# Kernel optimization log

Measured on AMD Instinct MI355X. Metric: run time of the kernel, lower is better.

## Reference

```python
import jax, jax.numpy as jnp
import numpy as np

H, W = 256, 336
FLOW_SCALING = float(max(H, W))  # max(config['loader']['resolution'])
REG_WEIGHT = 0.001               # config['loss']['flow_regul_weight']
B, N = 8, 262144


def setup_inputs() -> dict:
    key = jax.random.key(0)
    k1, k2, k3, k4, k5 = jax.random.split(key, 5)
    # small flow so a reasonable fraction of warped events stays in-bounds
    flow = 0.05 * jax.random.normal(k1, (B, 2, H, W), dtype=jnp.float32)
    ys = jax.random.randint(k2, (B, N), 0, H).astype(jnp.float32)
    xs = jax.random.randint(k3, (B, N), 0, W).astype(jnp.float32)
    ts = jax.random.uniform(k4, (B, N), dtype=jnp.float32)  # normalized timestamps in [0,1]
    pol = jax.random.randint(k5, (B, N), 0, 2)
    # event layout per the code: (ts, y, x, p)
    event_list = jnp.stack([ts, ys, xs, pol.astype(jnp.float32) * 2.0 - 1.0], axis=-1)
    pol_mask = jnp.stack([(pol == 1), (pol == 0)], axis=-1).astype(jnp.float32)  # [B,N,2]
    return {"flow": flow, "event_list": event_list, "pol_mask": pol_mask}


def _get_interpolation(events, event_flow, tref):
    # warped event coords (y, x): [B, N, 2]
    warped = events[:, :, 1:3] + (tref - events[:, :, 0:1]) * event_flow * FLOW_SCALING
    top_y = jnp.floor(warped[:, :, 0:1])
    bot_y = jnp.floor(warped[:, :, 0:1] + 1.0)
    left_x = jnp.floor(warped[:, :, 1:2])
    right_x = jnp.floor(warped[:, :, 1:2] + 1.0)
    # four bilinear corners stacked along event dim -> [B, 4N, 2]
    idx = jnp.concatenate([
        jnp.concatenate([top_y, left_x], -1),
        jnp.concatenate([top_y, right_x], -1),
        jnp.concatenate([bot_y, left_x], -1),
        jnp.concatenate([bot_y, right_x], -1)], axis=1)
    warped4 = jnp.tile(warped, (1, 4, 1))
    weights = jnp.maximum(0.0, 1.0 - jnp.abs(warped4 - idx))
    mask = ((idx[:, :, 0:1] >= 0) & (idx[:, :, 0:1] < H)
            & (idx[:, :, 1:2] >= 0) & (idx[:, :, 1:2] < W)).astype(weights.dtype)
    idx = idx * mask          # unfeasible indices -> 0
    weights = weights * mask  # unfeasible weights -> 0
    flat_idx = (idx[:, :, 0] * W + idx[:, :, 1]).astype(jnp.int32)  # [B, 4N]
    w = jnp.prod(weights, axis=-1, keepdims=True)                    # [B, 4N, 1]
    return flat_idx, w


def _interpolate(flat_idx, weights, polarity_mask):
    # scatter-add bilinear weights into an H*W image, per batch element
    w = (weights * polarity_mask)[:, :, 0]  # [B, 4N]
    return jax.vmap(lambda i, v: jax.ops.segment_sum(v, i, num_segments=H * W))(flat_idx, w)


def reference(flow, event_list, pol_mask):
    pol4 = jnp.tile(pol_mask, (1, 4, 1))              # [B, 4N, 2]
    ts4 = jnp.tile(event_list[:, :, 0:1], (1, 4, 1))  # [B, 4N, 1]
    # gather flow at original event pixel locations
    flow_idx = (event_list[:, :, 1] * W + event_list[:, :, 2]).astype(jnp.int32)  # [B, N]
    flow_flat = flow.reshape(flow.shape[0], 2, -1)
    event_flowy = jnp.take_along_axis(flow_flat[:, 1, :], flow_idx, axis=1)
    event_flowx = jnp.take_along_axis(flow_flat[:, 0, :], flow_idx, axis=1)
    event_flow = jnp.stack([event_flowy, event_flowx], axis=-1)  # [B, N, 2] (y, x)

    loss = jnp.float32(0.0)
    # forward warp (tref=1, avg ts) and backward warp (tref=0, avg 1-ts)
    for tref, tgrad in ((1.0, ts4), (0.0, 1.0 - ts4)):
        idx, wts = _get_interpolation(event_list, event_flow, tref)
        for p in range(2):  # positive / negative polarity
            pm = pol4[:, :, p:p + 1]
            iwe = _interpolate(idx, wts, pm)
            iwe_ts = _interpolate(idx, wts * tgrad, pm)
            loss = loss + jnp.sum((iwe_ts / (iwe + 1e-9)) ** 2)

    # charbonnier flow smoothness
    flow_dx = flow[:, :, :-1, :] - flow[:, :, 1:, :]
    flow_dy = flow[:, :, :, :-1] - flow[:, :, :, 1:]
    smooth = jnp.sum(jnp.sqrt(flow_dx ** 2 + 1e-6)) + jnp.sum(jnp.sqrt(flow_dy ** 2 + 1e-6))
    return loss + REG_WEIGHT * smooth
```

## Files before the change

### kernel.cpp

```cpp
#include <hip/hip_runtime.h>

#define HH 256
#define WW 336
#define HWPIX (HH * WW)
#define BATCH 8
#define NEV 262144
#define NEV_SHIFT 18
#define FLOW_SCALING 336.0f
#define REG_WEIGHT 0.001f

#define BANDS 32
#define BANDSHIFT 3
#define BANDROWS 8
#define NBINS (2 * BATCH * BANDS)
#define CAP 14336
#define GSTRIDE 16

#define BE_THREADS 512
#define EVPT 2
#define EV_PER_BLOCK (BE_THREADS * EVPT)
#define MAXITEMS 4096

#define HTILE (BANDROWS * WW)
#define NBLK_ACC NBINS

#define GCOUNT_BYTES (NBINS * GSTRIDE * 4)
#define ITEMS_BYTES ((size_t)NBINS * CAP * 8)

__device__ __forceinline__ float wave_reduce_sum(float v) {
    #pragma unroll
    for (int o = 32; o > 0; o >>= 1) v += __shfl_down(v, o, 64);
    return v;
}

__device__ __forceinline__ float charb(float d) { return sqrtf(d * d + 1e-6f); }

__global__ __launch_bounds__(256)
void flow_prep(const float* __restrict__ flow,
               unsigned int* __restrict__ gcount, float* __restrict__ loss_acc,
               unsigned int* __restrict__ done_count,
               float* __restrict__ smooth_partial) {
    __shared__ float red[4];
    int tid = threadIdx.x;
    if (blockIdx.x == 0) {
        for (int i = tid; i < NBINS * GSTRIDE; i += 256) gcount[i] = 0u;
        if (tid == 0) { *loss_acc = 0.0f; *done_count = 0u; }
    }

    const int N4 = BATCH * HWPIX / 4;
    const int H4 = HWPIX / 4;
    const int W4 = WW / 4;
    float v = 0.0f;
    for (int i = blockIdx.x * 256 + tid; i < N4; i += gridDim.x * 256) {
        int b = i / H4, u = i - b * H4;
        int row = u / W4, c4 = u - row * W4;
        const float4* ch0 = (const float4*)(flow + (size_t)b * 2 * HWPIX);
        const float4* ch1 = ch0 + H4;
        float4 a0 = ch0[u];
        float4 a1 = ch1[u];

        if (row < HH - 1) {
            float4 d0 = ch0[u + W4];
            float4 d1 = ch1[u + W4];
            v += charb(a0.x - d0.x) + charb(a0.y - d0.y) +
                 charb(a0.z - d0.z) + charb(a0.w - d0.w) +
                 charb(a1.x - d1.x) + charb(a1.y - d1.y) +
                 charb(a1.z - d1.z) + charb(a1.w - d1.w);
        }
        v += charb(a0.x - a0.y) + charb(a0.y - a0.z) + charb(a0.z - a0.w) +
             charb(a1.x - a1.y) + charb(a1.y - a1.z) + charb(a1.z - a1.w);
        if (c4 < W4 - 1) {
            float r0 = ((const float*)ch0)[4 * u + 4];
            float r1 = ((const float*)ch1)[4 * u + 4];
            v += charb(a0.w - r0) + charb(a1.w - r1);
        }
    }
    v = wave_reduce_sum(v);
    if ((tid & 63) == 0) red[tid >> 6] = v;
    __syncthreads();
    if (tid < 4) {
        float r = red[tid];
        r += __shfl_down(r, 2, 64);
        r += __shfl_down(r, 1, 64);
        if (tid == 0) smooth_partial[blockIdx.x] = r;
    }
}

__global__ __launch_bounds__(BE_THREADS)
void bin_events(const float* __restrict__ flow,
                const float4* __restrict__ ev,
                unsigned int* __restrict__ gcount,
                uint2* __restrict__ items) {
    __shared__ int lcnt[64];
    __shared__ int loff[64];
    __shared__ int gbase[64];
    __shared__ int stotal;
    __shared__ __align__(16) unsigned long long sval[MAXITEMS];

    int tid = threadIdx.x;
    if (tid < 64) lcnt[tid] = 0;
    __syncthreads();

    int base = blockIdx.x * EV_PER_BLOCK;
    int b = base >> NEV_SHIFT;
    const float* fxp = flow + (size_t)b * 2 * HWPIX;
    const float* fyp = fxp + HWPIX;

    unsigned int pkv[EVPT][2];
    unsigned int hiA[EVPT][2], hiB[EVPT][2];
    int rkA[EVPT][2], rkB[EVPT][2];

    #pragma unroll
    for (int e = 0; e < EVPT; ++e) {
        int bn = base + e * BE_THREADS + tid;
        float4 ee = ev[bn];
        float t = ee.x, y = ee.y, x = ee.z;
        unsigned int p = (ee.w > 0.0f) ? 0u : 1u;

        int iy = (int)y, ix = (int)x;
        int off = iy * WW + ix;
        float fx = fxp[off];
        float fy = fyp[off];

        #pragma unroll
        for (int tr = 0; tr < 2; ++tr) {
            rkA[e][tr] = -1; rkB[e][tr] = -1;
            float tref  = tr ? 0.0f : 1.0f;
            float tg    = tr ? (1.0f - t) : t;
            float dtS = (tref - t) * FLOW_SCALING;
            float wy = fmaf(dtS, fy, y);
            float wx = fmaf(dtS, fx, x);
            if (!(wx > -1.0f && wx < (float)WW)) continue;
            if (!(wy > -1.0f && wy < (float)HH)) continue;

            int ty = (int)floorf(wy);
            int band0 = -1, band1 = -1;
            if (ty >= 0 && ty < HH) band0 = ty >> BANDSHIFT;
            int r1 = ty + 1;
            if (r1 >= 0 && r1 < HH) {
                int bb = r1 >> BANDSHIFT;
                if (bb != band0) band1 = bb;
            }

            unsigned int qx = (unsigned int)(fmaf(wx, 2048.0f, 2048.5f));
            unsigned int qt = (unsigned int)(tg * 2047.0f + 0.5f);
            pkv[e][tr] = (qx << 12) | (qt << 1) | p;

            if (band0 >= 0) {
                float wyrel = wy - (float)(band0 * BANDROWS - 1);
                unsigned int qy = (unsigned int)fmaf(wyrel, 2048.0f, 0.5f);
                int lb = tr * BANDS + band0;
                hiA[e][tr] = qy | ((unsigned int)lb << 16);
                rkA[e][tr] = atomicAdd(&lcnt[lb], 1);
            }
            if (band1 >= 0) {
                float wyrel = wy - (float)(band1 * BANDROWS - 1);
                unsigned int qy = (unsigned int)fmaf(wyrel, 2048.0f, 0.5f);
                int lb = tr * BANDS + band1;
                hiB[e][tr] = qy | ((unsigned int)lb << 16);
                rkB[e][tr] = atomicAdd(&lcnt[lb], 1);
            }
        }
    }
    __syncthreads();

    if (tid < 64) {
        int c = lcnt[tid];
        int xg = c;
        #pragma unroll
        for (int o = 1; o < 64; o <<= 1) {
            int yv = __shfl_up(xg, o, 64);
            if (tid >= o) xg += yv;
        }
        loff[tid] = xg - c;
        if (tid == 63) stotal = xg;
        int gbin = ((tid >> 5) * BATCH + b) * BANDS + (tid & 31);
        gbase[tid] = c > 0 ? (int)atomicAdd(&gcount[gbin * GSTRIDE],
                                            (unsigned int)c) : 0;
    }
    __syncthreads();

    #pragma unroll
    for (int e = 0; e < EVPT; ++e) {
        #pragma unroll
        for (int tr = 0; tr < 2; ++tr) {
            if (rkA[e][tr] >= 0) {
                int lb = (hiA[e][tr] >> 16) & 63;
                sval[loff[lb] + rkA[e][tr]] =
                    (unsigned long long)pkv[e][tr] |
                    ((unsigned long long)hiA[e][tr] << 32);
            }
            if (rkB[e][tr] >= 0) {
                int lb = (hiB[e][tr] >> 16) & 63;
                sval[loff[lb] + rkB[e][tr]] =
                    (unsigned long long)pkv[e][tr] |
                    ((unsigned long long)hiB[e][tr] << 32);
            }
        }
    }
    __syncthreads();

    int total = stotal;
    for (int i = tid * 2; i < total; i += 2 * BE_THREADS) {
        uint4 two = *(const uint4*)&sval[i];
        unsigned int pk0 = two.x, h0 = two.y;
        unsigned int qy0 = h0 & 0xffffu;
        int lb0 = (h0 >> 16) & 63;
        int gs0 = gbase[lb0] + (i - loff[lb0]);
        int gbin0 = ((lb0 >> 5) * BATCH + b) * BANDS + (lb0 & 31);

        if ((i + 1) < total) {
            unsigned int pk1 = two.z, h1 = two.w;
            unsigned int qy1 = h1 & 0xffffu;
            int lb1 = (h1 >> 16) & 63;
            int gs1 = gbase[lb1] + (i + 1 - loff[lb1]);
            if (lb1 == lb0 && (gs0 & 1) == 0 && gs1 < CAP) {
                *(uint4*)(items + (size_t)gbin0 * CAP + gs0) =
                    make_uint4(pk0, qy0, pk1, qy1);
                continue;
            }
            int gbin1 = ((lb1 >> 5) * BATCH + b) * BANDS + (lb1 & 31);
            if (gs1 < CAP) items[(size_t)gbin1 * CAP + gs1] = make_uint2(pk1, qy1);
        }
        if (gs0 < CAP) items[(size_t)gbin0 * CAP + gs0] = make_uint2(pk0, qy0);
    }
}

__device__ __forceinline__ unsigned int pack_w(float w, float tg) {
    unsigned int lo16 = (unsigned int)fmaf(w, 1024.0f, 0.5f);
    unsigned int hi16 = (unsigned int)fmaf(w * tg, 1024.0f, 0.5f);
    return lo16 | (hi16 << 16);
}

__device__ __forceinline__ void accum_item(unsigned int* __restrict__ sA,
                                           unsigned int* __restrict__ sB,
                                           unsigned int pk, unsigned int qy) {
    float wx = (float)(pk >> 12) * (1.0f / 2048.0f) - 1.0f;
    float tg = (float)((pk >> 1) & 2047u) * (1.0f / 2047.0f);
    int p = pk & 1u;

    int rowq = qy >> 11;
    float fy = (float)(qy & 2047u) * (1.0f / 2048.0f);
    int row_top = rowq - 1;

    float lxf = floorf(wx);
    float fxx = wx - lxf;
    int lx = (int)lxf;

    unsigned int* A  = sA + p * HTILE;
    unsigned int* Bb = sB + p * HTILE;

    #pragma unroll
    for (int a = 0; a < 2; ++a) {
        int ry = row_top + a;
        if ((unsigned)ry >= (unsigned)BANDROWS) continue;
        float wrow = a ? fy : (1.0f - fy);
        int rb = ry * WW;
        if (lx >= 0 && lx + 1 < WW) {
            unsigned int pl = pack_w(wrow * (1.0f - fxx), tg);
            unsigned int pr = pack_w(wrow * fxx, tg);
            unsigned long long v =
                (unsigned long long)pl | ((unsigned long long)pr << 32);
            if ((lx & 1) == 0) {
                atomicAdd((unsigned long long*)(A + rb + lx), v);
            } else {
                atomicAdd((unsigned long long*)(Bb + rb + lx - 1), v);
            }
        } else if (lx == -1) {
            atomicAdd(&A[rb], pack_w(wrow * fxx, tg));
        } else if (lx == WW - 1) {
            atomicAdd(&A[rb + lx], pack_w(wrow * (1.0f - fxx), tg));
        }
    }
}

__global__ __launch_bounds__(1024)
void bin_accum(const unsigned int* __restrict__ gcount,
               const uint2* __restrict__ items,
               const float* __restrict__ smooth_partial,
               float* __restrict__ loss_acc,
               unsigned int* __restrict__ done_count,
               float* __restrict__ out) {
    __shared__ __align__(16) unsigned int sA[2 * HTILE];
    __shared__ __align__(16) unsigned int sB[2 * HTILE];
    __shared__ float red[16];
    __shared__ int lastflag;

    int band = blockIdx.x;
    int tr   = blockIdx.y;
    int b    = blockIdx.z;
    int tid  = threadIdx.x;

    for (int i = tid; i < 2 * HTILE; i += 1024) { sA[i] = 0u; sB[i] = 0u; }
    __syncthreads();

    int gbin = (tr * BATCH + b) * BANDS + band;
    int cnt = min((int)gcount[gbin * GSTRIDE], CAP);
    const uint2* bp = items + (size_t)gbin * CAP;
    const uint4* bp4 = (const uint4*)bp;

    int nquad = cnt >> 2;
    for (int n = tid; n < nquad; n += 1024) {
        uint4 c0 = bp4[2 * n];
        uint4 c1 = bp4[2 * n + 1];
        accum_item(sA, sB, c0.x, c0.y);
        accum_item(sA, sB, c0.z, c0.w);
        accum_item(sA, sB, c1.x, c1.y);
        accum_item(sA, sB, c1.z, c1.w);
    }
    int rem = cnt & 3;
    if (tid < rem) {
        uint2 u = bp[nquad * 4 + tid];
        accum_item(sA, sB, u.x, u.y);
    }
    __syncthreads();

    float v = 0.0f;
    for (int i = tid; i < 2 * HTILE; i += 1024) {
        int px = i - (i / WW) * WW;
        unsigned int u = sA[i] + (px ? sB[i - 1] : 0u);
        float iwe = (float)(u & 0xffffu);
        float its = (float)(u >> 16);
        float r = its / (iwe + 1.024e-6f);
        v += r * r;
    }
    v = wave_reduce_sum(v);
    if ((tid & 63) == 0) red[tid >> 6] = v;
    __syncthreads();
    if (tid == 0) {
        float r = 0.0f;
        #pragma unroll
        for (int k = 0; k < 16; ++k) r += red[k];
        atomicAdd(loss_acc, r);
        __threadfence();
        unsigned int t = atomicAdd(done_count, 1u);
        lastflag = (t == (unsigned)(NBLK_ACC - 1));
    }
    __syncthreads();

    if (lastflag) {
        float pv = (tid < 512) ? smooth_partial[tid] : 0.0f;
        pv = wave_reduce_sum(pv);
        if ((tid & 63) == 0) red[tid >> 6] = pv;
        __syncthreads();
        if (tid == 0) {
            float sm = 0.0f;
            #pragma unroll
            for (int k = 0; k < 16; ++k) sm += red[k];
            float total = atomicAdd(loss_acc, 0.0f);
            *out = total + REG_WEIGHT * sm;
        }
    }
}

extern "C" void kernel_launch(void* const* d_in, const int* in_sizes, int n_in,
                              void* d_out, int out_size, void* d_ws, size_t ws_size,
                              hipStream_t stream) {
    const float*  flow  = (const float*)d_in[0];
    const float4* ev    = (const float4*)d_in[1];
    float* out = (float*)d_out;

    unsigned int* gcount     = (unsigned int*)d_ws;
    float*        loss_acc   = (float*)((char*)d_ws + GCOUNT_BYTES);
    unsigned int* done_count = (unsigned int*)((char*)d_ws + GCOUNT_BYTES + 4);
    float*        smooth_p   = (float*)((char*)d_ws + GCOUNT_BYTES + 512);
    uint2*        items      = (uint2*)((char*)d_ws + GCOUNT_BYTES + 4096);

    flow_prep<<<512, 256, 0, stream>>>(flow, gcount, loss_acc,
                                       done_count, smooth_p);

    int total_ev = BATCH * NEV;
    bin_events<<<total_ev / EV_PER_BLOCK, BE_THREADS, 0, stream>>>(
        flow, ev, gcount, items);

    dim3 g2(BANDS, 2, BATCH);
    bin_accum<<<g2, 1024, 0, stream>>>(gcount, items, smooth_p, loss_acc,
                                       done_count, out);
}
```

Measured before the change: 149.1 us.

## Interleave flow channels, enlarge binning blocks, software-prefetch accumulation loads

flow_prep now also writes an interleaved (x,y) float2 copy of the flow into workspace, so bin_events fetches both components of an event's flow with one 8-byte gather instead of two scattered 4-byte loads. bin_events doubles its block size and shared item buffer (1024 threads, 8192 items). bin_accum's item loop is software-pipelined so the next quad of items is loaded before the current one is accumulated. The cost is an extra flow-sized write per call, more shared memory per binning block, and possibly lower occupancy.

Result: faster. 136.2 us (-8.7%).

```diff
diff --git a/kernel.cpp b/kernel.cpp
--- a/kernel.cpp
+++ b/kernel.cpp
@@ -16,10 +16,10 @@
 #define CAP 14336
 #define GSTRIDE 16
 
-#define BE_THREADS 512
+#define BE_THREADS 1024
 #define EVPT 2
 #define EV_PER_BLOCK (BE_THREADS * EVPT)
-#define MAXITEMS 4096
+#define MAXITEMS 8192
 
 #define HTILE (BANDROWS * WW)
 #define NBLK_ACC NBINS
@@ -36,7 +36,7 @@
 __device__ __forceinline__ float charb(float d) { return sqrtf(d * d + 1e-6f); }
 
 __global__ __launch_bounds__(256)
-void flow_prep(const float* __restrict__ flow,
+void flow_prep(const float* __restrict__ flow, float2* __restrict__ flowi,
                unsigned int* __restrict__ gcount, float* __restrict__ loss_acc,
                unsigned int* __restrict__ done_count,
                float* __restrict__ smooth_partial) {
@@ -59,6 +59,10 @@
         float4 a0 = ch0[u];
         float4 a1 = ch1[u];
 
+        float4* fo = (float4*)(flowi + (size_t)b * HWPIX);
+        fo[2 * u]     = make_float4(a0.x, a1.x, a0.y, a1.y);
+        fo[2 * u + 1] = make_float4(a0.z, a1.z, a0.w, a1.w);
+
         if (row < HH - 1) {
             float4 d0 = ch0[u + W4];
             float4 d1 = ch1[u + W4];
@@ -87,7 +91,7 @@
 }
 
 __global__ __launch_bounds__(BE_THREADS)
-void bin_events(const float* __restrict__ flow,
+void bin_events(const float2* __restrict__ flowi,
                 const float4* __restrict__ ev,
                 unsigned int* __restrict__ gcount,
                 uint2* __restrict__ items) {
@@ -103,8 +107,7 @@
 
     int base = blockIdx.x * EV_PER_BLOCK;
     int b = base >> NEV_SHIFT;
-    const float* fxp = flow + (size_t)b * 2 * HWPIX;
-    const float* fyp = fxp + HWPIX;
+    const float2* fB = flowi + (size_t)b * HWPIX;
 
     unsigned int pkv[EVPT][2];
     unsigned int hiA[EVPT][2], hiB[EVPT][2];
@@ -118,9 +121,8 @@
         unsigned int p = (ee.w > 0.0f) ? 0u : 1u;
 
         int iy = (int)y, ix = (int)x;
-        int off = iy * WW + ix;
-        float fx = fxp[off];
-        float fy = fyp[off];
+        float2 f = fB[iy * WW + ix];
+        float fx = f.x, fy = f.y;
 
         #pragma unroll
         for (int tr = 0; tr < 2; ++tr) {
@@ -300,9 +302,18 @@
     const uint4* bp4 = (const uint4*)bp;
 
     int nquad = cnt >> 2;
-    for (int n = tid; n < nquad; n += 1024) {
-        uint4 c0 = bp4[2 * n];
-        uint4 c1 = bp4[2 * n + 1];
+    if (tid < nquad) {
+        uint4 c0 = bp4[2 * tid];
+        uint4 c1 = bp4[2 * tid + 1];
+        for (int n = tid + 1024; n < nquad; n += 1024) {
+            uint4 d0 = bp4[2 * n];
+            uint4 d1 = bp4[2 * n + 1];
+            accum_item(sA, sB, c0.x, c0.y);
+            accum_item(sA, sB, c0.z, c0.w);
+            accum_item(sA, sB, c1.x, c1.y);
+            accum_item(sA, sB, c1.z, c1.w);
+            c0 = d0; c1 = d1;
+        }
         accum_item(sA, sB, c0.x, c0.y);
         accum_item(sA, sB, c0.z, c0.w);
         accum_item(sA, sB, c1.x, c1.y);
@@ -365,13 +376,14 @@
     unsigned int* done_count = (unsigned int*)((char*)d_ws + GCOUNT_BYTES + 4);
     float*        smooth_p   = (float*)((char*)d_ws + GCOUNT_BYTES + 512);
     uint2*        items      = (uint2*)((char*)d_ws + GCOUNT_BYTES + 4096);
-
-    flow_prep<<<512, 256, 0, stream>>>(flow, gcount, loss_acc,
+    float2*       flowi      = (float2*)((char*)d_ws + GCOUNT_BYTES + 4096 + ITEMS_BYTES);
+
+    flow_prep<<<512, 256, 0, stream>>>(flow, flowi, gcount, loss_acc,
                                        done_count, smooth_p);
 
     int total_ev = BATCH * NEV;
     bin_events<<<total_ev / EV_PER_BLOCK, BE_THREADS, 0, stream>>>(
-        flow, ev, gcount, items);
+        flowi, ev, gcount, items);
 
     dim3 g2(BANDS, 2, BATCH);
     bin_accum<<<g2, 1024, 0, stream>>>(gcount, items, smooth_p, loss_acc,
```
